# Optimization experiments

Hardware: AMD Instinct MI355X
Metric: run time of the kernel (lower is better)

The kernel has to match this reference:

```python
import jax, jax.numpy as jnp
import numpy as np

H = 1024        # hidden_size
E = 16          # n_routed_experts
K = 4           # num_experts_per_tok (top_k)
I = 512         # moe_intermediate_size
NS = 2          # n_shared_experts
IS = I * NS     # shared-expert intermediate size
N = 2048        # num_tokens
ROUTED_SCALE = 2.5  # routed_scaling_factor


def setup_inputs() -> dict:
    key = jax.random.key(0)
    ks = jax.random.split(key, 6)
    s = 0.02
    return {
        "hidden_states": jax.random.normal(ks[0], (N, H), jnp.float32),
        "gate_w": jax.random.normal(ks[1], (H, E), jnp.float32) * s,
        "w_gate_up": jax.random.normal(ks[2], (E, H, 2 * I), jnp.float32) * s,
        "w_down": jax.random.normal(ks[3], (E, I, H), jnp.float32) * s,
        "shared_gate_up": jax.random.normal(ks[4], (H, 2 * IS), jnp.float32) * s,
        "shared_down": jax.random.normal(ks[5], (IS, H), jnp.float32) * s,
    }


def _moe_forward(x, gate_w, w_gate_up, w_down, shared_gate_up, shared_down):
    n = x.shape[0]
    # --- router: sigmoid scoring + top-k (num_expert_group=topk_group=1) ---
    router_logits = x @ gate_w                      # [N, E]
    scores = jax.nn.sigmoid(router_logits)
    top_vals, top_idx = jax.lax.top_k(scores, K)    # [N, K]
    # renormalize (norm_topk_prob=True)
    top_w = top_vals / jnp.sum(top_vals, axis=-1, keepdims=True)
    # dense combine weights [N, E], zero outside top-k
    w_dense = jnp.zeros((n, E), x.dtype).at[jnp.arange(n)[:, None], top_idx].add(top_w)

    # --- routed experts: SwiGLU per expert, weighted combine ---
    gu = jnp.einsum("nh,ehf->nef", x, w_gate_up)    # [N, E, 2I]
    act = jax.nn.silu(gu[..., :I]) * gu[..., I:]    # SiluAndMul -> [N, E, I]
    routed = jnp.einsum("nei,eih,ne->nh", act, w_down, w_dense)  # [N, H]

    # --- shared experts MLP (WBLMLP) ---
    gus = x @ shared_gate_up                        # [N, 2*IS]
    shared = (jax.nn.silu(gus[:, :IS]) * gus[:, IS:]) @ shared_down  # [N, H]

    return routed * ROUTED_SCALE + shared


def reference(hidden_states, gate_w, w_gate_up, w_down, shared_gate_up, shared_down):
    return _moe_forward(hidden_states, gate_w, w_gate_up, w_down,
                        shared_gate_up, shared_down)
```

## Files before the change

### kernel.cpp

```cpp
#include <hip/hip_runtime.h>
#include <hip/hip_bf16.h>
#include <stdint.h>

#define NTOK 2048
#define HDIM 1024
#define NEXP 16
#define TOPK 4
#define IR   512
#define ISH  1024
#define RSCALE 2.5f

typedef short bf16x4 __attribute__((ext_vector_type(4)));
typedef short bf16x8 __attribute__((ext_vector_type(8)));
typedef float f32x4  __attribute__((ext_vector_type(4)));

static __device__ __forceinline__ unsigned short f2bf(float f){
  union { float fv; uint32_t u; } v; v.fv = f;
  uint32_t r = v.u + 0x7fffu + ((v.u >> 16) & 1u);
  return (unsigned short)(r >> 16);
}
static __device__ __forceinline__ float bf2f(unsigned short s){
  union { uint32_t u; float f; } v; v.u = ((uint32_t)s) << 16;
  return v.f;
}
static __device__ __forceinline__ unsigned int pkbf2(float lo, float hi){
  union { __hip_bfloat162 b; unsigned int u; } cv;
  cv.b = __float22bfloat162_rn(make_float2(lo, hi));
  return cv.u;
}

static __device__ __forceinline__ void gl_lds16(const void* gp, void* lp){
  __builtin_amdgcn_global_load_lds(
      (const __attribute__((address_space(1))) unsigned int*)gp,
      (__attribute__((address_space(3))) unsigned int*)lp, 16, 0, 0);
}

__global__ __launch_bounds__(256) void prep_kernel(
    const float* __restrict__ x, const float* __restrict__ gw,
    float* __restrict__ topkw, int* __restrict__ choice,
    unsigned short* __restrict__ xbf,
    const float* __restrict__ wgu, unsigned short* __restrict__ wgu_t,
    const float* __restrict__ wdn, unsigned short* __restrict__ wdn_t,
    const float* __restrict__ sgu, unsigned short* __restrict__ sgu_t,
    const float* __restrict__ sdn, unsigned short* __restrict__ sdn_t)
{
  __shared__ float tile[64 * 69];
  const int tid = threadIdx.x;
  const int bid = blockIdx.x;

  if (bid < 512){
    const int lane = tid & 63;
    const int t = bid * 4 + (tid >> 6);
    float s[NEXP];
    #pragma unroll
    for (int e = 0; e < NEXP; e++) s[e] = 0.f;
    #pragma unroll
    for (int j = 0; j < 8; j++){
      const int off = 128 * j + lane * 2;
      float2 xv = *(const float2*)(x + (size_t)t * HDIM + off);
      ushort2 xs = { f2bf(xv.x), f2bf(xv.y) };
      *(ushort2*)(xbf + (size_t)t * HDIM + off) = xs;
      const float4* g0 = (const float4*)(gw + (size_t)off * NEXP);
      const float4* g1 = (const float4*)(gw + (size_t)(off + 1) * NEXP);
      #pragma unroll
      for (int q = 0; q < 4; q++){
        float4 a = g0[q], b = g1[q];
        s[q * 4 + 0] += xv.x * a.x + xv.y * b.x;
        s[q * 4 + 1] += xv.x * a.y + xv.y * b.y;
        s[q * 4 + 2] += xv.x * a.z + xv.y * b.z;
        s[q * 4 + 3] += xv.x * a.w + xv.y * b.w;
      }
    }
    #pragma unroll
    for (int e = 0; e < NEXP; e++){
      #pragma unroll
      for (int off = 32; off; off >>= 1)
        s[e] += __shfl_xor(s[e], off);
    }
    float sc[NEXP];
    #pragma unroll
    for (int e = 0; e < NEXP; e++) sc[e] = 1.f / (1.f + __expf(-s[e]));
    unsigned mask = 0; float w[TOPK]; int id[TOPK];
    #pragma unroll
    for (int k = 0; k < TOPK; k++){
      float best = -1e30f; int bi = 0;
      #pragma unroll
      for (int e = 0; e < NEXP; e++){
        if (!((mask >> e) & 1u) && sc[e] > best){ best = sc[e]; bi = e; }
      }
      mask |= 1u << bi; id[k] = bi; w[k] = best;
    }
    float inv = 1.f / (w[0] + w[1] + w[2] + w[3]);
    if (lane == 0){
      #pragma unroll
      for (int k = 0; k < TOPK; k++){
        topkw[t * TOPK + k] = w[k] * inv;
        choice[t * TOPK + k] = id[k];
      }
    }
    return;
  }

  int id = bid - 512;
  const float* s; unsigned short* d; int R, C, rt, ct;
  if (id < 4096){
    int e = id >> 8, r = id & 255; rt = r >> 4; ct = r & 15;
    R = 1024; C = 1024; s = wgu + (size_t)e * 1048576; d = wgu_t + (size_t)e * 1048576;
  } else if (id < 6144){
    id -= 4096; int e = id >> 7, r = id & 127; rt = r >> 4; ct = r & 15;
    R = 512; C = 1024; s = wdn + (size_t)e * 524288; d = wdn_t + (size_t)e * 524288;
  } else if (id < 6656){
    id -= 6144; rt = id >> 5; ct = id & 31;
    R = 1024; C = 2048; s = sgu; d = sgu_t;
  } else {
    id -= 6656; rt = id >> 4; ct = id & 15;
    R = 1024; C = 1024; s = sdn; d = sdn_t;
  }
  const int r0 = rt * 64, c0 = ct * 64;
  #pragma unroll
  for (int i = 0; i < 4; i++){
    int r = i * 16 + (tid >> 4);
    int c = (tid & 15) * 4;
    float4 v = *(const float4*)(s + (size_t)(r0 + r) * C + c0 + c);
    *(float4*)(tile + r * 69 + c) = v;
  }
  __syncthreads();
  unsigned short* dt = d + ((size_t)ct * (R >> 6) + rt) * 4096;
  #pragma unroll
  for (int it = 0; it < 2; it++){
    int q = tid + it * 256;
    int c = q >> 3, rg = (q & 7) * 8;
    union { bf16x8 v; unsigned int u[4]; } pk;
    #pragma unroll
    for (int k = 0; k < 4; k++)
      pk.u[k] = pkbf2(tile[(rg + 2 * k) * 69 + c], tile[(rg + 2 * k + 1) * 69 + c]);
    *(bf16x8*)(dt + c * 64 + rg) = pk.v;
  }
}

__global__ __launch_bounds__(256) void build_lists(
    const int* __restrict__ choice, int* __restrict__ counts, int* __restrict__ lists)
{
  const int e = blockIdx.x;
  const int tid = threadIdx.x;
  __shared__ int scnt[256];
  const int base = tid * 32;
  unsigned m = 0; int local = 0;
  #pragma unroll
  for (int i = 0; i < 32; i++){
    bool hit = (choice[base + i] == e);
    m |= (unsigned)hit << i;
    local += hit;
  }
  scnt[tid] = local;
  __syncthreads();
  int v = local;
  for (int off = 1; off < 256; off <<= 1){
    int add = (tid >= off) ? scnt[tid - off] : 0;
    __syncthreads();
    v += add; scnt[tid] = v;
    __syncthreads();
  }
  int pos = v - local;
  #pragma unroll
  for (int i = 0; i < 32; i++){
    if ((m >> i) & 1u) lists[e * NTOK + pos++] = base + i;
  }
  if (tid == 255) counts[e] = v;
}

__global__ __launch_bounds__(256) void gu_gemm(
    const unsigned short* __restrict__ xbf, const unsigned short* __restrict__ wgu_t,
    const unsigned short* __restrict__ sgu_t,
    unsigned short* __restrict__ act_r, unsigned short* __restrict__ act_s,
    const int* __restrict__ lists, const int* __restrict__ counts)
{
  __shared__ unsigned short sA[2][128 * 32];
  __shared__ unsigned short sB[2][128 * 32];
  __shared__ int sAid[128];

  const int tid = threadIdx.x;
  const int L = blockIdx.x;
  const bool routed = (L < 512);
  int e, mIdx, n0, count, NPAIR, NCH;
  const unsigned short* Bt;
  unsigned short* act;
  if (routed){
    int p = L & 7, t = L >> 3;
    mIdx = t & 3; e = t >> 2; n0 = p * 64;
    count = counts[e]; NPAIR = IR; NCH = 4;
    Bt = wgu_t + (size_t)e * (2 * IR) * HDIM;
    act = act_r;
  } else {
    int v = L - 512;
    e = 0; n0 = (v & 15) * 64; mIdx = v >> 4;
    count = NTOK; NPAIR = ISH; NCH = 16;
    Bt = sgu_t; act = act_s;
  }

  const int wv = tid >> 6, lane = tid & 63, lr = lane & 15, g = lane >> 4;
  const int wm = wv >> 1, wn = wv & 1;

  const unsigned short* bsrc[2];
  #pragma unroll
  for (int it = 0; it < 2; it++){
    int q = tid + it * 256;
    int c = q >> 2, ko = (q & 3) * 8;
    int grp = c >> 5, within = c & 31;
    int grow = n0 + (grp >> 1) * 32 + within + ((grp & 1) ? NPAIR : 0);
    bsrc[it] = Bt + ((size_t)(grow >> 6) * (HDIM >> 6)) * 4096 + ((grow & 63) << 6) + ko;
  }

  for (int mt = mIdx; mt * 128 < count; mt += NCH){
    const int m0 = mt * 128;
    __syncthreads();
    if (tid < 128){
      int idx = m0 + tid;
      int aid;
      if (routed) aid = (idx < count) ? lists[e * NTOK + idx] : lists[e * NTOK];
      else        aid = idx;
      sAid[tid] = aid;
    }
    __syncthreads();
    const unsigned short* asrc[2];
    #pragma unroll
    for (int it = 0; it < 2; it++){
      int q = tid + it * 256;
      int r = q >> 2, ko = (q & 3) * 8;
      int aid = sAid[r];
      int tok = routed ? (aid >> 2) : aid;
      asrc[it] = xbf + (size_t)tok * HDIM + ko;
    }

    const f32x4 z4 = {0.f, 0.f, 0.f, 0.f};
    f32x4 acc[4][4];
    #pragma unroll
    for (int i = 0; i < 4; i++)
      #pragma unroll
      for (int j = 0; j < 4; j++) acc[i][j] = z4;

    for (int k0 = 0; k0 < HDIM; k0 += 64){
      const size_t bk = (size_t)k0 * 64;
      #pragma unroll
      for (int it = 0; it < 2; it++){
        gl_lds16(asrc[it] + k0,       sA[0] + (tid + it * 256) * 8);
        gl_lds16(asrc[it] + k0 + 32,  sA[1] + (tid + it * 256) * 8);
        gl_lds16(bsrc[it] + bk,       sB[0] + (tid + it * 256) * 8);
        gl_lds16(bsrc[it] + bk + 32,  sB[1] + (tid + it * 256) * 8);
      }
      __syncthreads();
      #pragma unroll
      for (int h = 0; h < 2; h++){
        bf16x8 af[4], bfr[4];
        #pragma unroll
        for (int i = 0; i < 4; i++){
          af[i]  = *(const bf16x8*)(sA[h] + (wm * 64 + i * 16 + lr) * 32 + g * 8);
          bfr[i] = *(const bf16x8*)(sB[h] + (wn * 64 + i * 16 + lr) * 32 + g * 8);
        }
        #pragma unroll
        for (int mi = 0; mi < 4; mi++)
          #pragma unroll
          for (int ni = 0; ni < 4; ni++)
            acc[mi][ni] = __builtin_amdgcn_mfma_f32_16x16x32_bf16(af[mi], bfr[ni], acc[mi][ni], 0, 0, 0);
      }
      __syncthreads();
    }

    #pragma unroll
    for (int mi = 0; mi < 4; mi++){
      #pragma unroll
      for (int r = 0; r < 4; r++){
        int row = wm * 64 + mi * 16 + g * 4 + r;
        if (routed && m0 + row >= count) continue;
        int aid = sAid[row];
        size_t arow = (size_t)aid * NPAIR;
        #pragma unroll
        for (int ni = 0; ni < 2; ni++){
          float gv = acc[mi][ni][r];
          float uv = acc[mi][ni + 2][r];
          float a = gv / (1.f + __expf(-gv)) * uv;
          act[arow + n0 + wn * 32 + ni * 16 + lr] = f2bf(a);
        }
      }
    }
  }
}

__global__ __launch_bounds__(256) void down_gemm(
    const unsigned short* __restrict__ act_r, const unsigned short* __restrict__ act_s,
    const unsigned short* __restrict__ wdn_t, const unsigned short* __restrict__ sdn_t,
    float* __restrict__ out, unsigned short* __restrict__ downout,
    const int* __restrict__ lists, const int* __restrict__ counts)
{
  __shared__ unsigned short sA[2][128 * 32];
  __shared__ unsigned short sB[2][128 * 32];
  __shared__ int sAid[128];

  const int tid = threadIdx.x;
  const int L = blockIdx.x;
  const bool routed = (L < 512);
  int e, mIdx, n0, count, K, NCH;
  const unsigned short* Bt;
  const unsigned short* Ab;
  if (routed){
    int p = L & 7, t = L >> 3;
    mIdx = t & 3; e = t >> 2; n0 = p * 128;
    count = counts[e]; K = IR; NCH = 4;
    Bt = wdn_t + (size_t)e * HDIM * IR;
    Ab = act_r;
  } else {
    int v = L - 512;
    e = 0; n0 = (v & 7) * 128; mIdx = v >> 3;
    count = NTOK; K = ISH; NCH = 16;
    Bt = sdn_t; Ab = act_s;
  }

  const int wv = tid >> 6, lane = tid & 63, lr = lane & 15, g = lane >> 4;
  const int wm = wv >> 1, wn = wv & 1;

  const unsigned short* bsrc[2];
  #pragma unroll
  for (int it = 0; it < 2; it++){
    int q = tid + it * 256;
    int c = q >> 2, ko = (q & 3) * 8;
    int grow = n0 + c;
    bsrc[it] = Bt + ((size_t)(grow >> 6) * (K >> 6)) * 4096 + ((grow & 63) << 6) + ko;
  }

  for (int mt = mIdx; mt * 128 < count; mt += NCH){
    const int m0 = mt * 128;
    __syncthreads();
    if (tid < 128){
      int idx = m0 + tid;
      int aid;
      if (routed) aid = (idx < count) ? lists[e * NTOK + idx] : lists[e * NTOK];
      else        aid = idx;
      sAid[tid] = aid;
    }
    __syncthreads();
    const unsigned short* asrc[2];
    #pragma unroll
    for (int it = 0; it < 2; it++){
      int q = tid + it * 256;
      int r = q >> 2, ko = (q & 3) * 8;
      asrc[it] = Ab + (size_t)sAid[r] * K + ko;
    }

    const f32x4 z4 = {0.f, 0.f, 0.f, 0.f};
    f32x4 acc[4][4];
    #pragma unroll
    for (int i = 0; i < 4; i++)
      #pragma unroll
      for (int j = 0; j < 4; j++) acc[i][j] = z4;

    for (int k0 = 0; k0 < K; k0 += 64){
      const size_t bk = (size_t)k0 * 64;
      #pragma unroll
      for (int it = 0; it < 2; it++){
        gl_lds16(asrc[it] + k0,       sA[0] + (tid + it * 256) * 8);
        gl_lds16(asrc[it] + k0 + 32,  sA[1] + (tid + it * 256) * 8);
        gl_lds16(bsrc[it] + bk,       sB[0] + (tid + it * 256) * 8);
        gl_lds16(bsrc[it] + bk + 32,  sB[1] + (tid + it * 256) * 8);
      }
      __syncthreads();
      #pragma unroll
      for (int h = 0; h < 2; h++){
        bf16x8 af[4], bfr[4];
        #pragma unroll
        for (int i = 0; i < 4; i++){
          af[i]  = *(const bf16x8*)(sA[h] + (wm * 64 + i * 16 + lr) * 32 + g * 8);
          bfr[i] = *(const bf16x8*)(sB[h] + (wn * 64 + i * 16 + lr) * 32 + g * 8);
        }
        #pragma unroll
        for (int mi = 0; mi < 4; mi++)
          #pragma unroll
          for (int ni = 0; ni < 4; ni++)
            acc[mi][ni] = __builtin_amdgcn_mfma_f32_16x16x32_bf16(af[mi], bfr[ni], acc[mi][ni], 0, 0, 0);
      }
      __syncthreads();
    }

    #pragma unroll
    for (int mi = 0; mi < 4; mi++){
      #pragma unroll
      for (int r = 0; r < 4; r++){
        int row = wm * 64 + mi * 16 + g * 4 + r;
        if (m0 + row >= count) continue;
        int aid = sAid[row];
        size_t orow = (size_t)aid * HDIM;
        if (routed){
          #pragma unroll
          for (int ni = 0; ni < 4; ni++)
            downout[orow + n0 + wn * 64 + ni * 16 + lr] = f2bf(acc[mi][ni][r]);
        } else {
          #pragma unroll
          for (int ni = 0; ni < 4; ni++)
            out[orow + n0 + wn * 64 + ni * 16 + lr] = acc[mi][ni][r];
        }
      }
    }
  }
}

__global__ __launch_bounds__(256) void combine_kernel(
    float* __restrict__ out, const unsigned short* __restrict__ downout,
    const float* __restrict__ topkw)
{
  const int idx = blockIdx.x * 256 + threadIdx.x;
  const int t = idx >> 8;
  const int c4 = (idx & 255) * 4;
  float4 o = *(float4*)(out + (size_t)t * HDIM + c4);
  float r0 = 0.f, r1 = 0.f, r2 = 0.f, r3 = 0.f;
  #pragma unroll
  for (int k = 0; k < TOPK; k++){
    float w = topkw[t * TOPK + k];
    const ushort4 dv = *(const ushort4*)(downout + (size_t)(t * TOPK + k) * HDIM + c4);
    r0 += w * bf2f(dv.x); r1 += w * bf2f(dv.y);
    r2 += w * bf2f(dv.z); r3 += w * bf2f(dv.w);
  }
  o.x += RSCALE * r0; o.y += RSCALE * r1; o.z += RSCALE * r2; o.w += RSCALE * r3;
  *(float4*)(out + (size_t)t * HDIM + c4) = o;
}

extern "C" void kernel_launch(void* const* d_in, const int* in_sizes, int n_in,
                              void* d_out, int out_size, void* d_ws, size_t ws_size,
                              hipStream_t stream) {
  const float* x   = (const float*)d_in[0];
  const float* gw  = (const float*)d_in[1];
  const float* wgu = (const float*)d_in[2];
  const float* wdn = (const float*)d_in[3];
  const float* sgu = (const float*)d_in[4];
  const float* sdn = (const float*)d_in[5];
  float* out = (float*)d_out;

  char* ws = (char*)d_ws;
  float* topkw = (float*)(ws + 0);
  int* choice  = (int*)(ws + 32768);
  int* counts  = (int*)(ws + 65536);
  int* lists   = (int*)(ws + 65792);
  unsigned short* xbf   = (unsigned short*)(ws + 197120);
  unsigned short* wgu_t = (unsigned short*)(ws + 197120 + 4194304ull);
  unsigned short* wdn_t = (unsigned short*)(ws + 197120 + 37748736ull);
  unsigned short* sgu_t = (unsigned short*)(ws + 197120 + 54525952ull);
  unsigned short* sdn_t = (unsigned short*)(ws + 197120 + 58720256ull);
  unsigned short* act_r = (unsigned short*)(ws + 197120 + 60817408ull);
  unsigned short* act_s = (unsigned short*)(ws + 197120 + 69206016ull);
  unsigned short* downout = wgu_t;

  prep_kernel<<<512 + 6912, 256, 0, stream>>>(x, gw, topkw, choice, xbf,
                                              wgu, wgu_t, wdn, wdn_t,
                                              sgu, sgu_t, sdn, sdn_t);
  build_lists<<<NEXP, 256, 0, stream>>>(choice, counts, lists);
  gu_gemm<<<768, 256, 0, stream>>>(xbf, wgu_t, sgu_t, act_r, act_s, lists, counts);
  down_gemm<<<640, 256, 0, stream>>>(act_r, act_s, wdn_t, sdn_t, out, downout, lists, counts);
  combine_kernel<<<(NTOK * HDIM / 4) / 256, 256, 0, stream>>>(out, downout, topkw);
}
```

Before: 132.7 us.

## Fuse down-projection weight fp32-to-bf16 conversion into down GEMM tile loads

```diff
diff --git a/kernel.cpp b/kernel.cpp
--- a/kernel.cpp
+++ b/kernel.cpp
@@ -40,9 +40,7 @@
     float* __restrict__ topkw, int* __restrict__ choice,
     unsigned short* __restrict__ xbf,
     const float* __restrict__ wgu, unsigned short* __restrict__ wgu_t,
-    const float* __restrict__ wdn, unsigned short* __restrict__ wdn_t,
-    const float* __restrict__ sgu, unsigned short* __restrict__ sgu_t,
-    const float* __restrict__ sdn, unsigned short* __restrict__ sdn_t)
+    const float* __restrict__ sgu, unsigned short* __restrict__ sgu_t)
 {
   __shared__ float tile[64 * 69];
   const int tid = threadIdx.x;
@@ -106,15 +104,9 @@
   if (id < 4096){
     int e = id >> 8, r = id & 255; rt = r >> 4; ct = r & 15;
     R = 1024; C = 1024; s = wgu + (size_t)e * 1048576; d = wgu_t + (size_t)e * 1048576;
-  } else if (id < 6144){
-    id -= 4096; int e = id >> 7, r = id & 127; rt = r >> 4; ct = r & 15;
-    R = 512; C = 1024; s = wdn + (size_t)e * 524288; d = wdn_t + (size_t)e * 524288;
-  } else if (id < 6656){
-    id -= 6144; rt = id >> 5; ct = id & 31;
+  } else {
+    id -= 4096; rt = id >> 5; ct = id & 31;
     R = 1024; C = 2048; s = sgu; d = sgu_t;
-  } else {
-    id -= 6656; rt = id >> 4; ct = id & 15;
-    R = 1024; C = 1024; s = sdn; d = sdn_t;
   }
   const int r0 = rt * 64, c0 = ct * 64;
   #pragma unroll
@@ -288,44 +280,39 @@
 
 __global__ __launch_bounds__(256) void down_gemm(
     const unsigned short* __restrict__ act_r, const unsigned short* __restrict__ act_s,
-    const unsigned short* __restrict__ wdn_t, const unsigned short* __restrict__ sdn_t,
-    float* __restrict__ out, unsigned short* __restrict__ downout,
+    const float* __restrict__ wdn, const float* __restrict__ sdn,
+    float* __restrict__ shout, unsigned short* __restrict__ downout,
     const int* __restrict__ lists, const int* __restrict__ counts)
 {
-  __shared__ unsigned short sA[2][128 * 32];
-  __shared__ unsigned short sB[2][128 * 32];
+  __shared__ unsigned short sA[128 * 64];
+  __shared__ unsigned short sB[128 * 64];
   __shared__ int sAid[128];
 
   const int tid = threadIdx.x;
   const int L = blockIdx.x;
   const bool routed = (L < 512);
   int e, mIdx, n0, count, K, NCH;
-  const unsigned short* Bt;
+  const float* Bsrc;
   const unsigned short* Ab;
   if (routed){
-    int p = L & 7, t = L >> 3;
-    mIdx = t & 3; e = t >> 2; n0 = p * 128;
+    e = L >> 5; int r = L & 31; mIdx = r >> 3; n0 = (r & 7) * 128;
     count = counts[e]; K = IR; NCH = 4;
-    Bt = wdn_t + (size_t)e * HDIM * IR;
+    Bsrc = wdn + (size_t)e * IR * HDIM;
     Ab = act_r;
   } else {
     int v = L - 512;
-    e = 0; n0 = (v & 7) * 128; mIdx = v >> 3;
+    e = 0; mIdx = v >> 3; n0 = (v & 7) * 128;
     count = NTOK; K = ISH; NCH = 16;
-    Bt = sdn_t; Ab = act_s;
+    Bsrc = sdn; Ab = act_s;
   }
 
   const int wv = tid >> 6, lane = tid & 63, lr = lane & 15, g = lane >> 4;
   const int wm = wv >> 1, wn = wv & 1;
-
-  const unsigned short* bsrc[2];
-  #pragma unroll
-  for (int it = 0; it < 2; it++){
-    int q = tid + it * 256;
-    int c = q >> 2, ko = (q & 3) * 8;
-    int grow = n0 + c;
-    bsrc[it] = Bt + ((size_t)(grow >> 6) * (K >> 6)) * 4096 + ((grow & 63) << 6) + ko;
-  }
+  const int sw = lr >> 1;
+
+  const int a = tid & 31, o = tid >> 5;
+  const int cbase = 4 * a;
+  const float* bthread = Bsrc + (size_t)(o * 8) * HDIM + n0 + 4 * a;
 
   for (int mt = mIdx; mt * 128 < count; mt += NCH){
     const int m0 = mt * 128;
@@ -338,12 +325,14 @@
       sAid[tid] = aid;
     }
     __syncthreads();
-    const unsigned short* asrc[2];
-    #pragma unroll
-    for (int it = 0; it < 2; it++){
-      int q = tid + it * 256;
-      int r = q >> 2, ko = (q & 3) * 8;
-      asrc[it] = Ab + (size_t)sAid[r] * K + ko;
+    const unsigned short* asrc[4];
+    unsigned short* adst[4];
+    #pragma unroll
+    for (int it = 0; it < 4; it++){
+      int s = tid + it * 256;
+      int row = s >> 3, j = s & 7;
+      asrc[it] = Ab + (size_t)sAid[row] * K + j * 8;
+      adst[it] = sA + row * 64 + (j ^ ((row >> 1) & 7)) * 8;
     }
 
     const f32x4 z4 = {0.f, 0.f, 0.f, 0.f};
@@ -354,13 +343,30 @@
       for (int j = 0; j < 4; j++) acc[i][j] = z4;
 
     for (int k0 = 0; k0 < K; k0 += 64){
-      const size_t bk = (size_t)k0 * 64;
-      #pragma unroll
-      for (int it = 0; it < 2; it++){
-        gl_lds16(asrc[it] + k0,       sA[0] + (tid + it * 256) * 8);
-        gl_lds16(asrc[it] + k0 + 32,  sA[1] + (tid + it * 256) * 8);
-        gl_lds16(bsrc[it] + bk,       sB[0] + (tid + it * 256) * 8);
-        gl_lds16(bsrc[it] + bk + 32,  sB[1] + (tid + it * 256) * 8);
+      bf16x8 av[4];
+      #pragma unroll
+      for (int it = 0; it < 4; it++)
+        av[it] = *(const bf16x8*)(asrc[it] + k0);
+      #pragma unroll
+      for (int it = 0; it < 4; it++)
+        *(bf16x8*)adst[it] = av[it];
+      float4 f[8];
+      const float* bp = bthread + (size_t)k0 * HDIM;
+      #pragma unroll
+      for (int r = 0; r < 8; r++)
+        f[r] = *(const float4*)(bp + (size_t)r * HDIM);
+      #pragma unroll
+      for (int i = 0; i < 4; i++){
+        union { bf16x8 v; unsigned int u[4]; } pk;
+        #pragma unroll
+        for (int rp = 0; rp < 4; rp++){
+          float lo = ((const float*)&f[2 * rp    ])[i];
+          float hi = ((const float*)&f[2 * rp + 1])[i];
+          pk.u[rp] = pkbf2(lo, hi);
+        }
+        int c = cbase + i;
+        int pos = o ^ ((c >> 1) & 7);
+        *(bf16x8*)(sB + c * 64 + pos * 8) = pk.v;
       }
       __syncthreads();
       #pragma unroll
@@ -368,8 +374,9 @@
         bf16x8 af[4], bfr[4];
         #pragma unroll
         for (int i = 0; i < 4; i++){
-          af[i]  = *(const bf16x8*)(sA[h] + (wm * 64 + i * 16 + lr) * 32 + g * 8);
-          bfr[i] = *(const bf16x8*)(sB[h] + (wn * 64 + i * 16 + lr) * 32 + g * 8);
+          int jx = ((h * 4 + g) ^ sw) * 8;
+          af[i]  = *(const bf16x8*)(sA + (wm * 64 + i * 16 + lr) * 64 + jx);
+          bfr[i] = *(const bf16x8*)(sB + (wn * 64 + i * 16 + lr) * 64 + jx);
         }
         #pragma unroll
         for (int mi = 0; mi < 4; mi++)
@@ -395,7 +402,7 @@
         } else {
           #pragma unroll
           for (int ni = 0; ni < 4; ni++)
-            out[orow + n0 + wn * 64 + ni * 16 + lr] = acc[mi][ni][r];
+            shout[orow + n0 + wn * 64 + ni * 16 + lr] = acc[mi][ni][r];
         }
       }
     }
@@ -403,13 +410,13 @@
 }
 
 __global__ __launch_bounds__(256) void combine_kernel(
-    float* __restrict__ out, const unsigned short* __restrict__ downout,
-    const float* __restrict__ topkw)
+    float* __restrict__ out, const float* __restrict__ shout,
+    const unsigned short* __restrict__ downout, const float* __restrict__ topkw)
 {
   const int idx = blockIdx.x * 256 + threadIdx.x;
   const int t = idx >> 8;
   const int c4 = (idx & 255) * 4;
-  float4 o = *(float4*)(out + (size_t)t * HDIM + c4);
+  float4 o = *(const float4*)(shout + (size_t)t * HDIM + c4);
   float r0 = 0.f, r1 = 0.f, r2 = 0.f, r3 = 0.f;
   #pragma unroll
   for (int k = 0; k < TOPK; k++){
@@ -440,18 +447,16 @@
   int* lists   = (int*)(ws + 65792);
   unsigned short* xbf   = (unsigned short*)(ws + 197120);
   unsigned short* wgu_t = (unsigned short*)(ws + 197120 + 4194304ull);
-  unsigned short* wdn_t = (unsigned short*)(ws + 197120 + 37748736ull);
-  unsigned short* sgu_t = (unsigned short*)(ws + 197120 + 54525952ull);
-  unsigned short* sdn_t = (unsigned short*)(ws + 197120 + 58720256ull);
-  unsigned short* act_r = (unsigned short*)(ws + 197120 + 60817408ull);
-  unsigned short* act_s = (unsigned short*)(ws + 197120 + 69206016ull);
+  unsigned short* sgu_t = (unsigned short*)(ws + 197120 + 37748736ull);
+  unsigned short* act_r = (unsigned short*)(ws + 197120 + 41943040ull);
+  unsigned short* act_s = (unsigned short*)(ws + 197120 + 50331648ull);
   unsigned short* downout = wgu_t;
-
-  prep_kernel<<<512 + 6912, 256, 0, stream>>>(x, gw, topkw, choice, xbf,
-                                              wgu, wgu_t, wdn, wdn_t,
-                                              sgu, sgu_t, sdn, sdn_t);
+  float*          shout   = (float*)((char*)wgu_t + 16777216ull);
+
+  prep_kernel<<<512 + 4608, 256, 0, stream>>>(x, gw, topkw, choice, xbf,
+                                              wgu, wgu_t, sgu, sgu_t);
   build_lists<<<NEXP, 256, 0, stream>>>(choice, counts, lists);
   gu_gemm<<<768, 256, 0, stream>>>(xbf, wgu_t, sgu_t, act_r, act_s, lists, counts);
-  down_gemm<<<640, 256, 0, stream>>>(act_r, act_s, wdn_t, sdn_t, out, downout, lists, counts);
-  combine_kernel<<<(NTOK * HDIM / 4) / 256, 256, 0, stream>>>(out, downout, topkw);
-}
+  down_gemm<<<640, 256, 0, stream>>>(act_r, act_s, wdn, sdn, shout, downout, lists, counts);
+  combine_kernel<<<(NTOK * HDIM / 4) / 256, 256, 0, stream>>>(out, shout, downout, topkw);
+}
```

Measured after the change: 132.0 us. About the same (-0.5%).

## Move down-proj weight conversion into gate-up GEMM launch to overlap

Applied to the files above, without the earlier changes.

```diff
diff --git a/kernel.cpp b/kernel.cpp
--- a/kernel.cpp
+++ b/kernel.cpp
@@ -35,16 +35,41 @@
       (__attribute__((address_space(3))) unsigned int*)lp, 16, 0, 0);
 }
 
+
+static __device__ __forceinline__ void conv_tile(
+    const float* __restrict__ s, unsigned short* __restrict__ d,
+    int R, int C, int rt, int ct, int tid, float* tile)
+{
+  const int r0 = rt * 64, c0 = ct * 64;
+  #pragma unroll
+  for (int i = 0; i < 4; i++){
+    int r = i * 16 + (tid >> 4);
+    int c = (tid & 15) * 4;
+    float4 v = *(const float4*)(s + (size_t)(r0 + r) * C + c0 + c);
+    *(float4*)(tile + r * 69 + c) = v;
+  }
+  __syncthreads();
+  unsigned short* dt = d + ((size_t)ct * (R >> 6) + rt) * 4096;
+  #pragma unroll
+  for (int it = 0; it < 2; it++){
+    int q = tid + it * 256;
+    int c = q >> 3, rg = (q & 7) * 8;
+    union { bf16x8 v; unsigned int u[4]; } pk;
+    #pragma unroll
+    for (int k = 0; k < 4; k++)
+      pk.u[k] = pkbf2(tile[(rg + 2 * k) * 69 + c], tile[(rg + 2 * k + 1) * 69 + c]);
+    *(bf16x8*)(dt + c * 64 + rg) = pk.v;
+  }
+}
+
 __global__ __launch_bounds__(256) void prep_kernel(
     const float* __restrict__ x, const float* __restrict__ gw,
     float* __restrict__ topkw, int* __restrict__ choice,
     unsigned short* __restrict__ xbf,
     const float* __restrict__ wgu, unsigned short* __restrict__ wgu_t,
-    const float* __restrict__ wdn, unsigned short* __restrict__ wdn_t,
-    const float* __restrict__ sgu, unsigned short* __restrict__ sgu_t,
-    const float* __restrict__ sdn, unsigned short* __restrict__ sdn_t)
-{
-  __shared__ float tile[64 * 69];
+    const float* __restrict__ sgu, unsigned short* __restrict__ sgu_t)
+{
+  __shared__ __align__(16) float tile[64 * 69];
   const int tid = threadIdx.x;
   const int bid = blockIdx.x;
 
@@ -102,39 +127,13 @@
   }
 
   int id = bid - 512;
-  const float* s; unsigned short* d; int R, C, rt, ct;
   if (id < 4096){
-    int e = id >> 8, r = id & 255; rt = r >> 4; ct = r & 15;
-    R = 1024; C = 1024; s = wgu + (size_t)e * 1048576; d = wgu_t + (size_t)e * 1048576;
-  } else if (id < 6144){
-    id -= 4096; int e = id >> 7, r = id & 127; rt = r >> 4; ct = r & 15;
-    R = 512; C = 1024; s = wdn + (size_t)e * 524288; d = wdn_t + (size_t)e * 524288;
-  } else if (id < 6656){
-    id -= 6144; rt = id >> 5; ct = id & 31;
-    R = 1024; C = 2048; s = sgu; d = sgu_t;
+    int e = id >> 8, r = id & 255;
+    conv_tile(wgu + (size_t)e * 1048576, wgu_t + (size_t)e * 1048576,
+              1024, 1024, r >> 4, r & 15, tid, tile);
   } else {
-    id -= 6656; rt = id >> 4; ct = id & 15;
-    R = 1024; C = 1024; s = sdn; d = sdn_t;
-  }
-  const int r0 = rt * 64, c0 = ct * 64;
-  #pragma unroll
-  for (int i = 0; i < 4; i++){
-    int r = i * 16 + (tid >> 4);
-    int c = (tid & 15) * 4;
-    float4 v = *(const float4*)(s + (size_t)(r0 + r) * C + c0 + c);
-    *(float4*)(tile + r * 69 + c) = v;
-  }
-  __syncthreads();
-  unsigned short* dt = d + ((size_t)ct * (R >> 6) + rt) * 4096;
-  #pragma unroll
-  for (int it = 0; it < 2; it++){
-    int q = tid + it * 256;
-    int c = q >> 3, rg = (q & 7) * 8;
-    union { bf16x8 v; unsigned int u[4]; } pk;
-    #pragma unroll
-    for (int k = 0; k < 4; k++)
-      pk.u[k] = pkbf2(tile[(rg + 2 * k) * 69 + c], tile[(rg + 2 * k + 1) * 69 + c]);
-    *(bf16x8*)(dt + c * 64 + rg) = pk.v;
+    id -= 4096;
+    conv_tile(sgu, sgu_t, 1024, 2048, id >> 5, id & 31, tid, tile);
   }
 }
 
@@ -169,18 +168,38 @@
   if (tid == 255) counts[e] = v;
 }
 
-__global__ __launch_bounds__(256) void gu_gemm(
+__global__ __launch_bounds__(256) void gu_plus(
     const unsigned short* __restrict__ xbf, const unsigned short* __restrict__ wgu_t,
     const unsigned short* __restrict__ sgu_t,
     unsigned short* __restrict__ act_r, unsigned short* __restrict__ act_s,
-    const int* __restrict__ lists, const int* __restrict__ counts)
-{
-  __shared__ unsigned short sA[2][128 * 32];
-  __shared__ unsigned short sB[2][128 * 32];
-  __shared__ int sAid[128];
-
+    const int* __restrict__ lists, const int* __restrict__ counts,
+    const float* __restrict__ wdn, unsigned short* __restrict__ wdn_t,
+    const float* __restrict__ sdn, unsigned short* __restrict__ sdn_t)
+{
+  __shared__ __align__(16) char smem[33280];
   const int tid = threadIdx.x;
   const int L = blockIdx.x;
+
+  if (L >= 768){
+    float* tile = (float*)smem;
+    int id = L - 768;
+    if (id < 2048){
+      int e = id >> 7, r = id & 127;
+      conv_tile(wdn + (size_t)e * 524288, wdn_t + (size_t)e * 524288,
+                512, 1024, r >> 4, r & 15, tid, tile);
+    } else {
+      id -= 2048;
+      conv_tile(sdn, sdn_t, 1024, 1024, id >> 4, id & 15, tid, tile);
+    }
+    return;
+  }
+
+  unsigned short* sA0 = (unsigned short*)smem;
+  unsigned short* sA1 = sA0 + 4096;
+  unsigned short* sB0 = sA1 + 4096;
+  unsigned short* sB1 = sB0 + 4096;
+  int* sAid = (int*)(smem + 32768);
+
   const bool routed = (L < 512);
   int e, mIdx, n0, count, NPAIR, NCH;
   const unsigned short* Bt;
@@ -243,19 +262,21 @@
       const size_t bk = (size_t)k0 * 64;
       #pragma unroll
       for (int it = 0; it < 2; it++){
-        gl_lds16(asrc[it] + k0,       sA[0] + (tid + it * 256) * 8);
-        gl_lds16(asrc[it] + k0 + 32,  sA[1] + (tid + it * 256) * 8);
-        gl_lds16(bsrc[it] + bk,       sB[0] + (tid + it * 256) * 8);
-        gl_lds16(bsrc[it] + bk + 32,  sB[1] + (tid + it * 256) * 8);
+        gl_lds16(asrc[it] + k0,       sA0 + (tid + it * 256) * 8);
+        gl_lds16(asrc[it] + k0 + 32,  sA1 + (tid + it * 256) * 8);
+        gl_lds16(bsrc[it] + bk,       sB0 + (tid + it * 256) * 8);
+        gl_lds16(bsrc[it] + bk + 32,  sB1 + (tid + it * 256) * 8);
       }
       __syncthreads();
       #pragma unroll
       for (int h = 0; h < 2; h++){
+        const unsigned short* sAh = h ? sA1 : sA0;
+        const unsigned short* sBh = h ? sB1 : sB0;
         bf16x8 af[4], bfr[4];
         #pragma unroll
         for (int i = 0; i < 4; i++){
-          af[i]  = *(const bf16x8*)(sA[h] + (wm * 64 + i * 16 + lr) * 32 + g * 8);
-          bfr[i] = *(const bf16x8*)(sB[h] + (wn * 64 + i * 16 + lr) * 32 + g * 8);
+          af[i]  = *(const bf16x8*)(sAh + (wm * 64 + i * 16 + lr) * 32 + g * 8);
+          bfr[i] = *(const bf16x8*)(sBh + (wn * 64 + i * 16 + lr) * 32 + g * 8);
         }
         #pragma unroll
         for (int mi = 0; mi < 4; mi++)
@@ -447,11 +468,11 @@
   unsigned short* act_s = (unsigned short*)(ws + 197120 + 69206016ull);
   unsigned short* downout = wgu_t;
 
-  prep_kernel<<<512 + 6912, 256, 0, stream>>>(x, gw, topkw, choice, xbf,
-                                              wgu, wgu_t, wdn, wdn_t,
-                                              sgu, sgu_t, sdn, sdn_t);
+  prep_kernel<<<512 + 4608, 256, 0, stream>>>(x, gw, topkw, choice, xbf,
+                                              wgu, wgu_t, sgu, sgu_t);
   build_lists<<<NEXP, 256, 0, stream>>>(choice, counts, lists);
-  gu_gemm<<<768, 256, 0, stream>>>(xbf, wgu_t, sgu_t, act_r, act_s, lists, counts);
+  gu_plus<<<768 + 2304, 256, 0, stream>>>(xbf, wgu_t, sgu_t, act_r, act_s,
+                                          lists, counts, wdn, wdn_t, sdn, sdn_t);
   down_gemm<<<640, 256, 0, stream>>>(act_r, act_s, wdn_t, sdn_t, out, downout, lists, counts);
   combine_kernel<<<(NTOK * HDIM / 4) / 256, 256, 0, stream>>>(out, downout, topkw);
 }
```

Result: faster. 129.6 us (-2.3%).
